# Kernel tuning notes

Measured on AMD Instinct MI355X. Metric: run time of the kernel, lower is better.

The kernel has to match this reference:

```python
import jax, jax.numpy as jnp
import numpy as np

N_NODES = 100000
N_EDGES = 1600000


def gcn_conv(x, row, col, norm, W, b, n_nodes):
    # PyG GCNConv: h = x @ W; aggregate normalized messages over (A + I); add bias
    h = x @ W                                   # [N, out]
    msg = h[col] * norm[:, None]                # [E+N, out] gather + scale
    out = jax.ops.segment_sum(msg, row, num_segments=n_nodes)  # scatter-add
    return out + b


def _norm_and_loops(edge_index, n_nodes):
    # add self-loops, compute symmetric normalization coefficients
    row = jnp.concatenate([edge_index[0], jnp.arange(n_nodes, dtype=edge_index.dtype)])
    col = jnp.concatenate([edge_index[1], jnp.arange(n_nodes, dtype=edge_index.dtype)])
    deg = jax.ops.segment_sum(jnp.ones_like(row, dtype=jnp.float32), row,
                              num_segments=n_nodes)
    dinv = jnp.where(deg > 0, jax.lax.rsqrt(deg), 0.0)
    norm = dinv[row] * dinv[col]
    return row, col, norm


def reference(x, edge_index, W1, b1, W2, b2, W3, b3):
    n_nodes = x.shape[0]
    row, col, norm = _norm_and_loops(edge_index, n_nodes)
    h = jax.nn.relu(gcn_conv(x, row, col, norm, W1, b1, n_nodes))
    h = jax.nn.relu(gcn_conv(h, row, col, norm, W2, b2, n_nodes))
    h = gcn_conv(h, row, col, norm, W3, b3, n_nodes)
    return jax.nn.log_softmax(h, axis=1)


def setup_inputs() -> dict:
    key = jax.random.key(0)
    ks = jax.random.split(key, 5)
    d_in, d_hid, d_out = 128, 128, 16
    x = jax.random.normal(ks[0], (N_NODES, d_in), dtype=jnp.float32)
    edge_index = jax.random.randint(ks[1], (2, N_EDGES), 0, N_NODES, dtype=jnp.int64)
    s1 = 1.0 / np.sqrt(d_in)
    s3 = 1.0 / np.sqrt(d_hid)
    W1 = jax.random.normal(ks[2], (d_in, d_hid), dtype=jnp.float32) * s1
    W2 = jax.random.normal(ks[3], (d_hid, d_hid), dtype=jnp.float32) * s3
    W3 = jax.random.normal(ks[4], (d_hid, d_out), dtype=jnp.float32) * s3
    return {
        "x": x, "edge_index": edge_index,
        "W1": W1, "b1": jnp.zeros((d_hid,), jnp.float32),
        "W2": W2, "b2": jnp.zeros((d_hid,), jnp.float32),
        "W3": W3, "b3": jnp.zeros((d_out,), jnp.float32),
    }
```

## Files before the change

kernel.cpp:

```cpp
#include <hip/hip_runtime.h>

typedef unsigned int u32;
typedef _Float16 f16;
typedef __attribute__((ext_vector_type(8))) _Float16 half8;
typedef __attribute__((ext_vector_type(2))) _Float16 half2_t;
typedef __attribute__((ext_vector_type(4))) float f32x4;

#define D_IN 128
#define D_HID 128
#define D_OUT 16
#define RPB 128
#define MAXBUCK 1024
#define CHUNK 16384
#define PGRAN 4
#define SLACK 2048


__global__ __launch_bounds__(256) void detect_k(const int* __restrict__ ei,
                                                u32* __restrict__ flag, int n) {
    int i = blockIdx.x * 256 + threadIdx.x;
    if (i < n && (i & 1) && ei[i] != 0) atomicOr(flag, 1u);
}

__device__ inline int load_row(const int* ei, u32 f, int e, int E) {
    return f ? ei[e] : ei[2 * e];
}
__device__ inline int load_col(const int* ei, u32 f, int e, int E) {
    return f ? ei[E + e] : ei[2 * E + 2 * e];
}
__device__ inline int clampi(int v, int n) {
    v = v < 0 ? 0 : v;
    return v >= n ? n - 1 : v;
}
__device__ inline u32 al16(u32 v) { return (v + 15u) & ~15u; }

__global__ __launch_bounds__(256) void hist_k(const int* __restrict__ ei,
                                              const u32* __restrict__ flag,
                                              u32* __restrict__ Hmat,
                                              int E, int N, int NBK, int NB) {
    __shared__ u32 lh[MAXBUCK];
    int tid = threadIdx.x;
    for (int i = tid; i < NBK; i += 256) lh[i] = 0;
    __syncthreads();
    u32 f = *flag;
    int base = blockIdx.x * CHUNK;
    int lim = base + CHUNK < E ? base + CHUNK : E;
    for (int e = base + tid; e < lim; e += 256) {
        int r = clampi(load_row(ei, f, e, E), N);
        atomicAdd(&lh[(u32)r >> 7], 1u);
    }
    __syncthreads();
    for (int i = tid; i < NBK; i += 256)
        Hmat[(size_t)i * NB + blockIdx.x] = lh[i];
}

__global__ __launch_bounds__(256) void scan1(const u32* __restrict__ cnt,
                                             u32* __restrict__ excl,
                                             u32* __restrict__ partial, int n) {
    __shared__ u32 sm[256];
    int tid = threadIdx.x;
    int i = blockIdx.x * 256 + tid;
    u32 v = (i < n) ? cnt[i] : 0u;
    sm[tid] = v;
    __syncthreads();
    for (int off = 1; off < 256; off <<= 1) {
        u32 t = (tid >= off) ? sm[tid - off] : 0u;
        __syncthreads();
        sm[tid] += t;
        __syncthreads();
    }
    if (i < n) excl[i] = sm[tid] - v;
    if (tid == 255) partial[blockIdx.x] = sm[255];
}

__global__ __launch_bounds__(512) void scan2(u32* __restrict__ partial, int nb) {
    __shared__ u32 sm[512];
    int tid = threadIdx.x;
    u32 v = (tid < nb) ? partial[tid] : 0u;
    sm[tid] = v;
    __syncthreads();
    for (int off = 1; off < 512; off <<= 1) {
        u32 t = (tid >= off) ? sm[tid - off] : 0u;
        __syncthreads();
        sm[tid] += t;
        __syncthreads();
    }
    if (tid < nb) partial[tid] = sm[tid] - v;
}

__global__ __launch_bounds__(256) void scan3(u32* __restrict__ excl,
                                             const u32* __restrict__ partial,
                                             int n, int E) {
    int i = blockIdx.x * 256 + threadIdx.x;
    if (i < n) excl[i] += partial[blockIdx.x];
    if (i == 0) excl[n] = (u32)E;
}

__global__ __launch_bounds__(256) void scatter_bd(const int* __restrict__ ei,
                                                  const u32* __restrict__ flag,
                                                  const u32* __restrict__ Hbase,
                                                  u32* __restrict__ bdata,
                                                  int E, int N, int NBK, int NB) {
    __shared__ u32 lbase[MAXBUCK];
    int tid = threadIdx.x;
    for (int i = tid; i < NBK; i += 256)
        lbase[i] = Hbase[(size_t)i * NB + blockIdx.x];
    __syncthreads();
    u32 f = *flag;
    int base = blockIdx.x * CHUNK;
    int lim = base + CHUNK < E ? base + CHUNK : E;
    for (int e = base + tid; e < lim; e += 256) {
        int r = clampi(load_row(ei, f, e, E), N);
        int c = clampi(load_col(ei, f, e, E), N);
        u32 pos = atomicAdd(&lbase[(u32)r >> 7], 1u);
        if (pos < (u32)E) bdata[pos] = ((u32)(r & (RPB - 1)) << 20) | (u32)c;
    }
}

__global__ __launch_bounds__(256) void finalize_k(const u32* __restrict__ bdata,
                                                  const u32* __restrict__ Hbase,
                                                  u32* __restrict__ row_start,
                                                  u32* __restrict__ rend,
                                                  float* __restrict__ dinv,
                                                  u32* __restrict__ ecol,
                                                  int N, int E, int NB) {
    __shared__ u32 smc[RPB];
    __shared__ u32 cur[RPB];
    int b = blockIdx.x;
    int tid = threadIdx.x;
    u32 s = Hbase[(size_t)b * NB];
    u32 t = Hbase[(size_t)(b + 1) * NB];
    u32 pbase = al16(s) + (u32)b * SLACK;
    if (tid < RPB) smc[tid] = 0;
    __syncthreads();
    for (u32 i = s + tid; i < t; i += 256)
        atomicAdd(&smc[bdata[i] >> 20], 1u);
    __syncthreads();
    u32 deg = (tid < RPB) ? smc[tid] : 0;
    u32 pdeg = (deg + PGRAN - 1) & ~(u32)(PGRAN - 1);
    if (tid < RPB) smc[tid] = pdeg;
    __syncthreads();
    for (int off = 1; off < RPB; off <<= 1) {
        u32 tv = (tid < RPB && tid >= off) ? smc[tid - off] : 0u;
        __syncthreads();
        if (tid < RPB) smc[tid] += tv;
        __syncthreads();
    }
    u32 pexcl = (tid < RPB) ? (smc[tid] - pdeg) : 0;
    if (tid < RPB) {
        int r = b * RPB + tid;
        if (r < N) {
            row_start[r] = pbase + pexcl;
            rend[r] = pbase + pexcl + pdeg;
            dinv[r] = rsqrtf((float)(deg + 1u));
        }
        cur[tid] = pbase + pexcl;
    }
    __syncthreads();
    for (u32 i = s + tid; i < t; i += 256) {
        u32 rec = bdata[i];
        u32 pos = atomicAdd(&cur[rec >> 20], 1u);
        ecol[pos] = rec & 0xFFFFFu;
    }
    __syncthreads();
    if (tid < RPB) {
        u32 st = pbase + pexcl;
        for (u32 k = deg; k < pdeg; k++) ecol[st + k] = (u32)N;
    }
}

__global__ __launch_bounds__(256) void reformat_all(const float* __restrict__ W1,
                                                    const float* __restrict__ W2,
                                                    const float* __restrict__ W3,
                                                    f16* __restrict__ W1h, f16* __restrict__ W1l,
                                                    f16* __restrict__ W2h, f16* __restrict__ W2l,
                                                    f16* __restrict__ W3h, f16* __restrict__ W3l,
                                                    f16* __restrict__ hzero,
                                                    f16* __restrict__ h3zero) {
    if (blockIdx.x == 17) {
        int tix = threadIdx.x;
        if (tix < 128) hzero[tix] = (f16)0;
        else if (tix < 144) h3zero[tix - 128] = (f16)0;
        return;
    }
    const float* W;
    f16 *Wh, *Wl;
    int ntiles, bidx;
    if (blockIdx.x < 8) { W = W1; Wh = W1h; Wl = W1l; ntiles = 8; bidx = blockIdx.x; }
    else if (blockIdx.x < 16) { W = W2; Wh = W2h; Wl = W2l; ntiles = 8; bidx = blockIdx.x - 8; }
    else { W = W3; Wh = W3h; Wl = W3l; ntiles = 1; bidx = 0; }
    int idx = bidx * 256 + threadIdx.x;
    int total = 4 * ntiles * 64;
    if (idx >= total) return;
    int lane = idx & 63;
    int st = idx >> 6;
    int t = st % ntiles;
    int s = st / ntiles;
    int Nc = ntiles * 16;
    int n = t * 16 + (lane & 15);
    int kb = lane >> 4;
    half8 vh, vl;
#pragma unroll
    for (int j = 0; j < 8; j++) {
        float w = W[(size_t)(s * 32 + kb * 8 + j) * Nc + n];
        f16 hi = (f16)w;
        f16 lo = (f16)(w - (float)hi);
        vh[j] = hi;
        vl[j] = lo;
    }
    *(half8*)(Wh + (size_t)idx * 8) = vh;
    *(half8*)(Wl + (size_t)idx * 8) = vl;
}


__global__ __launch_bounds__(256) void gemm128_l1(const float* __restrict__ A,
                                                  const f16* __restrict__ Wh,
                                                  const f16* __restrict__ Wl,
                                                  const float* __restrict__ dinv,
                                                  f16* __restrict__ H, int M) {
    int wave = threadIdx.x >> 6, lane = threadIdx.x & 63;
    int mbase = blockIdx.x * 64 + wave * 16;
    int mload = mbase + (lane & 15);
    if (mload >= M) mload = M - 1;
    int kq = lane >> 4;
    f32x4 acc[8];
#pragma unroll
    for (int t = 0; t < 8; t++) acc[t] = (f32x4){0.f, 0.f, 0.f, 0.f};
#pragma unroll
    for (int s = 0; s < 4; s++) {
        const float* ap = A + (size_t)mload * 128 + s * 32 + kq * 8;
        half8 ah, al;
#pragma unroll
        for (int j = 0; j < 8; j++) {
            float v = ap[j];
            f16 hi = (f16)v;
            ah[j] = hi;
            al[j] = (f16)(v - (float)hi);
        }
#pragma unroll
        for (int t = 0; t < 8; t++) {
            half8 bh = *(const half8*)(Wh + (size_t)((s * 8 + t) * 64 + lane) * 8);
            half8 bl = *(const half8*)(Wl + (size_t)((s * 8 + t) * 64 + lane) * 8);
            acc[t] = __builtin_amdgcn_mfma_f32_16x16x32_f16(ah, bh, acc[t], 0, 0, 0);
            acc[t] = __builtin_amdgcn_mfma_f32_16x16x32_f16(ah, bl, acc[t], 0, 0, 0);
            acc[t] = __builtin_amdgcn_mfma_f32_16x16x32_f16(al, bh, acc[t], 0, 0, 0);
        }
    }
    int coln = lane & 15;
    int rbase = mbase + ((lane >> 4) << 2);
    float dsc[4];
#pragma unroll
    for (int i = 0; i < 4; i++) {
        int rr = rbase + i;
        dsc[i] = dinv[rr < M ? rr : M - 1];
    }
#pragma unroll
    for (int t = 0; t < 8; t++) {
#pragma unroll
        for (int i = 0; i < 4; i++) {
            int rr = rbase + i;
            if (rr < M) H[(size_t)rr * 128 + t * 16 + coln] = (f16)(acc[t][i] * dsc[i]);
        }
    }
}

__global__ __launch_bounds__(256) void gemm128_l2(const f16* __restrict__ A,
                                                  const f16* __restrict__ Wh,
                                                  const f16* __restrict__ Wl,
                                                  f16* __restrict__ H, int M) {
    int wave = threadIdx.x >> 6, lane = threadIdx.x & 63;
    int mbase = blockIdx.x * 64 + wave * 16;
    int mload = mbase + (lane & 15);
    if (mload >= M) mload = M - 1;
    int kq = lane >> 4;
    f32x4 acc[8];
#pragma unroll
    for (int t = 0; t < 8; t++) acc[t] = (f32x4){0.f, 0.f, 0.f, 0.f};
#pragma unroll
    for (int s = 0; s < 4; s++) {
        half8 a = *(const half8*)(A + (size_t)mload * 128 + s * 32 + kq * 8);
#pragma unroll
        for (int t = 0; t < 8; t++) {
            half8 bh = *(const half8*)(Wh + (size_t)((s * 8 + t) * 64 + lane) * 8);
            half8 bl = *(const half8*)(Wl + (size_t)((s * 8 + t) * 64 + lane) * 8);
            acc[t] = __builtin_amdgcn_mfma_f32_16x16x32_f16(a, bh, acc[t], 0, 0, 0);
            acc[t] = __builtin_amdgcn_mfma_f32_16x16x32_f16(a, bl, acc[t], 0, 0, 0);
        }
    }
    int coln = lane & 15;
    int rbase = mbase + ((lane >> 4) << 2);
#pragma unroll
    for (int t = 0; t < 8; t++) {
#pragma unroll
        for (int i = 0; i < 4; i++) {
            int rr = rbase + i;
            if (rr < M) H[(size_t)rr * 128 + t * 16 + coln] = (f16)acc[t][i];
        }
    }
}

__global__ __launch_bounds__(256) void gemm16(const f16* __restrict__ A,
                                              const f16* __restrict__ Wh,
                                              const f16* __restrict__ Wl,
                                              f16* __restrict__ H, int M) {
    int wave = threadIdx.x >> 6, lane = threadIdx.x & 63;
    int mbase = blockIdx.x * 64 + wave * 16;
    int mload = mbase + (lane & 15);
    if (mload >= M) mload = M - 1;
    int kq = lane >> 4;
    f32x4 acc = (f32x4){0.f, 0.f, 0.f, 0.f};
#pragma unroll
    for (int s = 0; s < 4; s++) {
        half8 a = *(const half8*)(A + (size_t)mload * 128 + s * 32 + kq * 8);
        half8 bh = *(const half8*)(Wh + (size_t)(s * 64 + lane) * 8);
        half8 bl = *(const half8*)(Wl + (size_t)(s * 64 + lane) * 8);
        acc = __builtin_amdgcn_mfma_f32_16x16x32_f16(a, bh, acc, 0, 0, 0);
        acc = __builtin_amdgcn_mfma_f32_16x16x32_f16(a, bl, acc, 0, 0, 0);
    }
    int coln = lane & 15;
    int rbase = mbase + ((lane >> 4) << 2);
#pragma unroll
    for (int i = 0; i < 4; i++) {
        int rr = rbase + i;
        if (rr < M) H[(size_t)rr * 16 + coln] = (f16)acc[i];
    }
}

__global__ __launch_bounds__(256) void agg128(const f16* __restrict__ h,
                                              const u32* __restrict__ ecol,
                                              const u32* __restrict__ row_start,
                                              const u32* __restrict__ rend,
                                              const float* __restrict__ dinv,
                                              const float* __restrict__ bias,
                                              f16* __restrict__ out, int M) {
    int lane = threadIdx.x & 63;
    int wave = __builtin_amdgcn_readfirstlane(threadIdx.x >> 6);
    int r = blockIdx.x * 4 + wave;
    if (r >= M) return;
    u32 beg = (u32)__builtin_amdgcn_readfirstlane((int)row_start[r]);
    u32 end = (u32)__builtin_amdgcn_readfirstlane((int)rend[r]);
    float dr = dinv[r];
    const char* hb = (const char*)h;
    u32 loff = (u32)lane << 2;
    float ax0 = 0, ay0 = 0, ax1 = 0, ay1 = 0, ax2 = 0, ay2 = 0, ax3 = 0, ay3 = 0;
    u32 e = beg;
    for (; e + 16 <= end; e += 16) {
        const u32* ep = ecol + e;
        u32 c[16];
#pragma unroll
        for (int j = 0; j < 16; j++) c[j] = ep[j];
        half2_t v[16];
#pragma unroll
        for (int j = 0; j < 16; j++)
            v[j] = *(const half2_t*)(hb + ((c[j] << 8) + loff));
#pragma unroll
        for (int j = 0; j < 16; j += 4) {
            ax0 = fmaf((float)v[j][0],     dr, ax0); ay0 = fmaf((float)v[j][1],     dr, ay0);
            ax1 = fmaf((float)v[j + 1][0], dr, ax1); ay1 = fmaf((float)v[j + 1][1], dr, ay1);
            ax2 = fmaf((float)v[j + 2][0], dr, ax2); ay2 = fmaf((float)v[j + 2][1], dr, ay2);
            ax3 = fmaf((float)v[j + 3][0], dr, ax3); ay3 = fmaf((float)v[j + 3][1], dr, ay3);
        }
    }
    for (; e < end; e += 4) {
        const u32* ep = ecol + e;
        u32 c0 = ep[0], c1 = ep[1], c2 = ep[2], c3 = ep[3];
        half2_t v0 = *(const half2_t*)(hb + ((c0 << 8) + loff));
        half2_t v1 = *(const half2_t*)(hb + ((c1 << 8) + loff));
        half2_t v2 = *(const half2_t*)(hb + ((c2 << 8) + loff));
        half2_t v3 = *(const half2_t*)(hb + ((c3 << 8) + loff));
        ax0 = fmaf((float)v0[0], dr, ax0); ay0 = fmaf((float)v0[1], dr, ay0);
        ax1 = fmaf((float)v1[0], dr, ax1); ay1 = fmaf((float)v1[1], dr, ay1);
        ax2 = fmaf((float)v2[0], dr, ax2); ay2 = fmaf((float)v2[1], dr, ay2);
        ax3 = fmaf((float)v3[0], dr, ax3); ay3 = fmaf((float)v3[1], dr, ay3);
    }
    half2_t vs = *(const half2_t*)(hb + (((u32)r << 8) + loff));
    float2 bb = ((const float2*)bias)[lane];
    float ax = ((ax0 + ax1) + (ax2 + ax3)) + fmaf((float)vs[0], dr, bb.x);
    float ay = ((ay0 + ay1) + (ay2 + ay3)) + fmaf((float)vs[1], dr, bb.y);
    ax = fmaxf(ax, 0.f) * dr;
    ay = fmaxf(ay, 0.f) * dr;
    half2_t o;
    o[0] = (f16)ax;
    o[1] = (f16)ay;
    ((half2_t*)out)[(size_t)r * 64 + lane] = o;
}

__global__ __launch_bounds__(256) void agg16_lsm(const f16* __restrict__ h3,
                                                 const u32* __restrict__ ecol,
                                                 const u32* __restrict__ row_start,
                                                 const u32* __restrict__ rend,
                                                 const float* __restrict__ dinv,
                                                 const float* __restrict__ bias,
                                                 float* __restrict__ out, int M) {
    int g = threadIdx.x >> 4, l = threadIdx.x & 15;
    int r = blockIdx.x * 16 + g;
    if (r >= M) return;
    u32 beg = row_start[r], end = rend[r];
    float a0 = 0.f, a1 = 0.f, a2 = 0.f, a3 = 0.f;
    u32 e = beg;
    for (; e + 8 <= end; e += 8) {
        u32 c[8];
#pragma unroll
        for (int j = 0; j < 8; j++) c[j] = ecol[e + j];
        f16 v[8];
#pragma unroll
        for (int j = 0; j < 8; j++) v[j] = h3[(size_t)c[j] * 16 + l];
        a0 += (float)v[0] + (float)v[4];
        a1 += (float)v[1] + (float)v[5];
        a2 += (float)v[2] + (float)v[6];
        a3 += (float)v[3] + (float)v[7];
    }
    if (e < end) {
        u32 c[4];
#pragma unroll
        for (int j = 0; j < 4; j++) c[j] = ecol[e + j];
        f16 v[4];
#pragma unroll
        for (int j = 0; j < 4; j++) v[j] = h3[(size_t)c[j] * 16 + l];
        a0 += (float)v[0];
        a1 += (float)v[1];
        a2 += (float)v[2];
        a3 += (float)v[3];
    }
    float dr = dinv[r];
    float acc = (((a0 + a1) + (a2 + a3)) + (float)h3[(size_t)r * 16 + l]) * dr +
                bias[l];
    float m = acc;
#pragma unroll
    for (int o = 8; o >= 1; o >>= 1) m = fmaxf(m, __shfl_xor(m, o, 16));
    float ex = expf(acc - m);
    float s = ex;
#pragma unroll
    for (int o = 8; o >= 1; o >>= 1) s += __shfl_xor(s, o, 16);
    out[(size_t)r * 16 + l] = acc - m - logf(s);
}


extern "C" void kernel_launch(void* const* d_in, const int* in_sizes, int n_in,
                              void* d_out, int out_size, void* d_ws, size_t ws_size,
                              hipStream_t stream) {
    const float* x = (const float*)d_in[0];
    const int* ei = (const int*)d_in[1];
    const float* W1 = (const float*)d_in[2];
    const float* b1 = (const float*)d_in[3];
    const float* W2 = (const float*)d_in[4];
    const float* b2 = (const float*)d_in[5];
    const float* W3 = (const float*)d_in[6];
    const float* b3 = (const float*)d_in[7];
    int N = in_sizes[0] / D_IN;
    int E = in_sizes[1] / 2;

    int NBK = (N + RPB - 1) / RPB;
    int NB = (E + CHUNK - 1) / CHUNK;
    int L = NBK * NB;
    size_t Epad = ((size_t)E + 16) + (size_t)NBK * SLACK + 256;

    char* p = (char*)d_ws;
    auto alloc = [&](size_t bytes) -> void* {
        void* q = (void*)p;
        p += (bytes + 255) & ~(size_t)255;
        return q;
    };
    u32* flag = (u32*)alloc(256);
    float* dinv = (float*)alloc((size_t)N * 4);
    u32* row_start = (u32*)alloc((size_t)(N + 1) * 4);
    u32* rend = (u32*)alloc((size_t)N * 4);
    u32* partial2 = (u32*)alloc(4096);
    u32* Hmat = (u32*)alloc((size_t)(L + 1) * 4);
    u32* ecol = (u32*)alloc(Epad * 4);
    u32* bdata = (u32*)alloc((size_t)E * 4);
    f16* wf1h = (f16*)alloc(16384 * 2);
    f16* wf1l = (f16*)alloc(16384 * 2);
    f16* wf2h = (f16*)alloc(16384 * 2);
    f16* wf2l = (f16*)alloc(16384 * 2);
    f16* wf3h = (f16*)alloc(2048 * 2);
    f16* wf3l = (f16*)alloc(2048 * 2);
    f16* h = (f16*)alloc((size_t)(N + 1) * 128 * 2);
    f16* act = (f16*)alloc((size_t)N * 128 * 2);
    f16* h3 = (f16*)alloc((size_t)(N + 1) * 16 * 2);
    (void)ws_size; (void)n_in; (void)out_size;

    hipMemsetAsync(flag, 0, 4, stream);

    int nb2 = (L + 255) / 256;

    detect_k<<<32, 256, 0, stream>>>(ei, flag, 8192);
    hist_k<<<NB, 256, 0, stream>>>(ei, flag, Hmat, E, N, NBK, NB);
    scan1<<<nb2, 256, 0, stream>>>(Hmat, Hmat, partial2, L);
    scan2<<<1, 512, 0, stream>>>(partial2, nb2);
    scan3<<<nb2, 256, 0, stream>>>(Hmat, partial2, L, E);
    scatter_bd<<<NB, 256, 0, stream>>>(ei, flag, Hmat, bdata, E, N, NBK, NB);
    finalize_k<<<NBK, 256, 0, stream>>>(bdata, Hmat, row_start, rend, dinv,
                                        ecol, N, E, NB);

    reformat_all<<<18, 256, 0, stream>>>(W1, W2, W3, wf1h, wf1l, wf2h, wf2l,
                                         wf3h, wf3l,
                                         h + (size_t)N * 128,
                                         h3 + (size_t)N * 16);

    int gb = (N + 63) / 64;
    int ab = (N + 3) / 4;
    gemm128_l1<<<gb, 256, 0, stream>>>(x, wf1h, wf1l, dinv, h, N);
    agg128<<<ab, 256, 0, stream>>>(h, ecol, row_start, rend, dinv, b1, act, N);
    gemm128_l2<<<gb, 256, 0, stream>>>(act, wf2h, wf2l, h, N);
    agg128<<<ab, 256, 0, stream>>>(h, ecol, row_start, rend, dinv, b2, act, N);
    gemm16<<<gb, 256, 0, stream>>>(act, wf3h, wf3l, h3, N);
    agg16_lsm<<<(N + 15) / 16, 256, 0, stream>>>(h3, ecol, row_start, rend,
                                                 dinv, b3, (float*)d_out, N);
}
```

Baseline: 383.3 us.

## Stage GEMM weights in LDS, batch edge loads, pack row descriptors

Several independent tweaks. The hist and scatter kernels use a smaller CHUNK and unroll four edge loads per iteration to raise memory-level parallelism. The three GEMM kernels copy the split-f16 weights into shared memory and hoist activation loads ahead of the MFMA loop. Row start and end are packed into one uint2 descriptor, and the self and bias loads in the aggregation kernels are moved earlier. The trade-off is heavy LDS use in the 128-wide GEMMs (64KB per block), which may reduce occupancy.

```diff
diff --git a/kernel.cpp b/kernel.cpp
--- a/kernel.cpp
+++ b/kernel.cpp
@@ -11,7 +11,7 @@
 #define D_OUT 16
 #define RPB 128
 #define MAXBUCK 1024
-#define CHUNK 16384
+#define CHUNK 10240
 #define PGRAN 4
 #define SLACK 2048
 
@@ -45,9 +45,16 @@
     u32 f = *flag;
     int base = blockIdx.x * CHUNK;
     int lim = base + CHUNK < E ? base + CHUNK : E;
-    for (int e = base + tid; e < lim; e += 256) {
-        int r = clampi(load_row(ei, f, e, E), N);
-        atomicAdd(&lh[(u32)r >> 7], 1u);
+    for (int e = base + tid; e < lim; e += 1024) {
+        int e1 = e + 256, e2 = e + 512, e3 = e + 768;
+        int r0 = clampi(load_row(ei, f, e, E), N);
+        int r1 = (e1 < lim) ? clampi(load_row(ei, f, e1, E), N) : -1;
+        int r2 = (e2 < lim) ? clampi(load_row(ei, f, e2, E), N) : -1;
+        int r3 = (e3 < lim) ? clampi(load_row(ei, f, e3, E), N) : -1;
+        atomicAdd(&lh[(u32)r0 >> 7], 1u);
+        if (r1 >= 0) atomicAdd(&lh[(u32)r1 >> 7], 1u);
+        if (r2 >= 0) atomicAdd(&lh[(u32)r2 >> 7], 1u);
+        if (r3 >= 0) atomicAdd(&lh[(u32)r3 >> 7], 1u);
     }
     __syncthreads();
     for (int i = tid; i < NBK; i += 256)
@@ -109,18 +116,34 @@
     u32 f = *flag;
     int base = blockIdx.x * CHUNK;
     int lim = base + CHUNK < E ? base + CHUNK : E;
-    for (int e = base + tid; e < lim; e += 256) {
-        int r = clampi(load_row(ei, f, e, E), N);
-        int c = clampi(load_col(ei, f, e, E), N);
-        u32 pos = atomicAdd(&lbase[(u32)r >> 7], 1u);
-        if (pos < (u32)E) bdata[pos] = ((u32)(r & (RPB - 1)) << 20) | (u32)c;
+    for (int e = base + tid; e < lim; e += 1024) {
+        int e1 = e + 256, e2 = e + 512, e3 = e + 768;
+        int r0 = clampi(load_row(ei, f, e, E), N);
+        int c0 = clampi(load_col(ei, f, e, E), N);
+        int r1 = -1, c1 = 0, r2 = -1, c2 = 0, r3 = -1, c3 = 0;
+        if (e1 < lim) { r1 = clampi(load_row(ei, f, e1, E), N); c1 = clampi(load_col(ei, f, e1, E), N); }
+        if (e2 < lim) { r2 = clampi(load_row(ei, f, e2, E), N); c2 = clampi(load_col(ei, f, e2, E), N); }
+        if (e3 < lim) { r3 = clampi(load_row(ei, f, e3, E), N); c3 = clampi(load_col(ei, f, e3, E), N); }
+        u32 pos = atomicAdd(&lbase[(u32)r0 >> 7], 1u);
+        if (pos < (u32)E) bdata[pos] = ((u32)(r0 & (RPB - 1)) << 20) | (u32)c0;
+        if (r1 >= 0) {
+            pos = atomicAdd(&lbase[(u32)r1 >> 7], 1u);
+            if (pos < (u32)E) bdata[pos] = ((u32)(r1 & (RPB - 1)) << 20) | (u32)c1;
+        }
+        if (r2 >= 0) {
+            pos = atomicAdd(&lbase[(u32)r2 >> 7], 1u);
+            if (pos < (u32)E) bdata[pos] = ((u32)(r2 & (RPB - 1)) << 20) | (u32)c2;
+        }
+        if (r3 >= 0) {
+            pos = atomicAdd(&lbase[(u32)r3 >> 7], 1u);
+            if (pos < (u32)E) bdata[pos] = ((u32)(r3 & (RPB - 1)) << 20) | (u32)c3;
+        }
     }
 }
 
 __global__ __launch_bounds__(256) void finalize_k(const u32* __restrict__ bdata,
                                                   const u32* __restrict__ Hbase,
-                                                  u32* __restrict__ row_start,
-                                                  u32* __restrict__ rend,
+                                                  uint2* __restrict__ rdesc,
                                                   float* __restrict__ dinv,
                                                   u32* __restrict__ ecol,
                                                   int N, int E, int NB) {
@@ -150,8 +173,7 @@
     if (tid < RPB) {
         int r = b * RPB + tid;
         if (r < N) {
-            row_start[r] = pbase + pexcl;
-            rend[r] = pbase + pexcl + pdeg;
+            rdesc[r] = make_uint2(pbase + pexcl, pbase + pexcl + pdeg);
             dinv[r] = rsqrtf((float)(deg + 1u));
         }
         cur[tid] = pbase + pexcl;
@@ -218,29 +240,46 @@
                                                   const f16* __restrict__ Wl,
                                                   const float* __restrict__ dinv,
                                                   f16* __restrict__ H, int M) {
+    __shared__ f16 sBh[2048 * 8];
+    __shared__ f16 sBl[2048 * 8];
+    for (int i = threadIdx.x; i < 2048; i += 256) {
+        *(half8*)(sBh + (size_t)i * 8) = *(const half8*)(Wh + (size_t)i * 8);
+        *(half8*)(sBl + (size_t)i * 8) = *(const half8*)(Wl + (size_t)i * 8);
+    }
     int wave = threadIdx.x >> 6, lane = threadIdx.x & 63;
     int mbase = blockIdx.x * 64 + wave * 16;
     int mload = mbase + (lane & 15);
     if (mload >= M) mload = M - 1;
     int kq = lane >> 4;
-    f32x4 acc[8];
-#pragma unroll
-    for (int t = 0; t < 8; t++) acc[t] = (f32x4){0.f, 0.f, 0.f, 0.f};
+    f32x4 a0[4], a1[4];
 #pragma unroll
     for (int s = 0; s < 4; s++) {
         const float* ap = A + (size_t)mload * 128 + s * 32 + kq * 8;
+        a0[s] = *(const f32x4*)ap;
+        a1[s] = *(const f32x4*)(ap + 4);
+    }
+    f32x4 acc[8];
+#pragma unroll
+    for (int t = 0; t < 8; t++) acc[t] = (f32x4){0.f, 0.f, 0.f, 0.f};
+    __syncthreads();
+#pragma unroll
+    for (int s = 0; s < 4; s++) {
         half8 ah, al;
 #pragma unroll
-        for (int j = 0; j < 8; j++) {
-            float v = ap[j];
+        for (int j = 0; j < 4; j++) {
+            float v = a0[s][j];
             f16 hi = (f16)v;
             ah[j] = hi;
             al[j] = (f16)(v - (float)hi);
+            float w = a1[s][j];
+            f16 wi = (f16)w;
+            ah[j + 4] = wi;
+            al[j + 4] = (f16)(w - (float)wi);
         }
 #pragma unroll
         for (int t = 0; t < 8; t++) {
-            half8 bh = *(const half8*)(Wh + (size_t)((s * 8 + t) * 64 + lane) * 8);
-            half8 bl = *(const half8*)(Wl + (size_t)((s * 8 + t) * 64 + lane) * 8);
+            half8 bh = *(const half8*)(sBh + (size_t)((s * 8 + t) * 64 + lane) * 8);
+            half8 bl = *(const half8*)(sBl + (size_t)((s * 8 + t) * 64 + lane) * 8);
             acc[t] = __builtin_amdgcn_mfma_f32_16x16x32_f16(ah, bh, acc[t], 0, 0, 0);
             acc[t] = __builtin_amdgcn_mfma_f32_16x16x32_f16(ah, bl, acc[t], 0, 0, 0);
             acc[t] = __builtin_amdgcn_mfma_f32_16x16x32_f16(al, bh, acc[t], 0, 0, 0);
@@ -268,23 +307,33 @@
                                                   const f16* __restrict__ Wh,
                                                   const f16* __restrict__ Wl,
                                                   f16* __restrict__ H, int M) {
+    __shared__ f16 sBh[2048 * 8];
+    __shared__ f16 sBl[2048 * 8];
+    for (int i = threadIdx.x; i < 2048; i += 256) {
+        *(half8*)(sBh + (size_t)i * 8) = *(const half8*)(Wh + (size_t)i * 8);
+        *(half8*)(sBl + (size_t)i * 8) = *(const half8*)(Wl + (size_t)i * 8);
+    }
     int wave = threadIdx.x >> 6, lane = threadIdx.x & 63;
     int mbase = blockIdx.x * 64 + wave * 16;
     int mload = mbase + (lane & 15);
     if (mload >= M) mload = M - 1;
     int kq = lane >> 4;
+    half8 a[4];
+#pragma unroll
+    for (int s = 0; s < 4; s++)
+        a[s] = *(const half8*)(A + (size_t)mload * 128 + s * 32 + kq * 8);
     f32x4 acc[8];
 #pragma unroll
     for (int t = 0; t < 8; t++) acc[t] = (f32x4){0.f, 0.f, 0.f, 0.f};
+    __syncthreads();
 #pragma unroll
     for (int s = 0; s < 4; s++) {
-        half8 a = *(const half8*)(A + (size_t)mload * 128 + s * 32 + kq * 8);
 #pragma unroll
         for (int t = 0; t < 8; t++) {
-            half8 bh = *(const half8*)(Wh + (size_t)((s * 8 + t) * 64 + lane) * 8);
-            half8 bl = *(const half8*)(Wl + (size_t)((s * 8 + t) * 64 + lane) * 8);
-            acc[t] = __builtin_amdgcn_mfma_f32_16x16x32_f16(a, bh, acc[t], 0, 0, 0);
-            acc[t] = __builtin_amdgcn_mfma_f32_16x16x32_f16(a, bl, acc[t], 0, 0, 0);
+            half8 bh = *(const half8*)(sBh + (size_t)((s * 8 + t) * 64 + lane) * 8);
+            half8 bl = *(const half8*)(sBl + (size_t)((s * 8 + t) * 64 + lane) * 8);
+            acc[t] = __builtin_amdgcn_mfma_f32_16x16x32_f16(a[s], bh, acc[t], 0, 0, 0);
+            acc[t] = __builtin_amdgcn_mfma_f32_16x16x32_f16(a[s], bl, acc[t], 0, 0, 0);
         }
     }
     int coln = lane & 15;
@@ -303,19 +352,30 @@
                                               const f16* __restrict__ Wh,
                                               const f16* __restrict__ Wl,
                                               f16* __restrict__ H, int M) {
+    __shared__ f16 sBh[256 * 8];
+    __shared__ f16 sBl[256 * 8];
+    if (threadIdx.x < 256) {
+        int i = threadIdx.x;
+        *(half8*)(sBh + (size_t)i * 8) = *(const half8*)(Wh + (size_t)i * 8);
+        *(half8*)(sBl + (size_t)i * 8) = *(const half8*)(Wl + (size_t)i * 8);
+    }
     int wave = threadIdx.x >> 6, lane = threadIdx.x & 63;
     int mbase = blockIdx.x * 64 + wave * 16;
     int mload = mbase + (lane & 15);
     if (mload >= M) mload = M - 1;
     int kq = lane >> 4;
+    half8 a[4];
+#pragma unroll
+    for (int s = 0; s < 4; s++)
+        a[s] = *(const half8*)(A + (size_t)mload * 128 + s * 32 + kq * 8);
     f32x4 acc = (f32x4){0.f, 0.f, 0.f, 0.f};
+    __syncthreads();
 #pragma unroll
     for (int s = 0; s < 4; s++) {
-        half8 a = *(const half8*)(A + (size_t)mload * 128 + s * 32 + kq * 8);
-        half8 bh = *(const half8*)(Wh + (size_t)(s * 64 + lane) * 8);
-        half8 bl = *(const half8*)(Wl + (size_t)(s * 64 + lane) * 8);
-        acc = __builtin_amdgcn_mfma_f32_16x16x32_f16(a, bh, acc, 0, 0, 0);
-        acc = __builtin_amdgcn_mfma_f32_16x16x32_f16(a, bl, acc, 0, 0, 0);
+        half8 bh = *(const half8*)(sBh + (size_t)(s * 64 + lane) * 8);
+        half8 bl = *(const half8*)(sBl + (size_t)(s * 64 + lane) * 8);
+        acc = __builtin_amdgcn_mfma_f32_16x16x32_f16(a[s], bh, acc, 0, 0, 0);
+        acc = __builtin_amdgcn_mfma_f32_16x16x32_f16(a[s], bl, acc, 0, 0, 0);
     }
     int coln = lane & 15;
     int rbase = mbase + ((lane >> 4) << 2);
@@ -328,8 +388,7 @@
 
 __global__ __launch_bounds__(256) void agg128(const f16* __restrict__ h,
                                               const u32* __restrict__ ecol,
-                                              const u32* __restrict__ row_start,
-                                              const u32* __restrict__ rend,
+                                              const uint2* __restrict__ rdesc,
                                               const float* __restrict__ dinv,
                                               const float* __restrict__ bias,
                                               f16* __restrict__ out, int M) {
@@ -337,13 +396,15 @@
     int wave = __builtin_amdgcn_readfirstlane(threadIdx.x >> 6);
     int r = blockIdx.x * 4 + wave;
     if (r >= M) return;
-    u32 beg = (u32)__builtin_amdgcn_readfirstlane((int)row_start[r]);
-    u32 end = (u32)__builtin_amdgcn_readfirstlane((int)rend[r]);
+    uint2 d = rdesc[r];
+    u32 e = (u32)__builtin_amdgcn_readfirstlane((int)d.x);
+    u32 end = (u32)__builtin_amdgcn_readfirstlane((int)d.y);
     float dr = dinv[r];
     const char* hb = (const char*)h;
     u32 loff = (u32)lane << 2;
+    float2 bb = ((const float2*)bias)[lane];
+    half2_t vs = *(const half2_t*)(hb + (((u32)r << 8) + loff));
     float ax0 = 0, ay0 = 0, ax1 = 0, ay1 = 0, ax2 = 0, ay2 = 0, ax3 = 0, ay3 = 0;
-    u32 e = beg;
     for (; e + 16 <= end; e += 16) {
         const u32* ep = ecol + e;
         u32 c[16];
@@ -373,8 +434,6 @@
         ax2 = fmaf((float)v2[0], dr, ax2); ay2 = fmaf((float)v2[1], dr, ay2);
         ax3 = fmaf((float)v3[0], dr, ax3); ay3 = fmaf((float)v3[1], dr, ay3);
     }
-    half2_t vs = *(const half2_t*)(hb + (((u32)r << 8) + loff));
-    float2 bb = ((const float2*)bias)[lane];
     float ax = ((ax0 + ax1) + (ax2 + ax3)) + fmaf((float)vs[0], dr, bb.x);
     float ay = ((ay0 + ay1) + (ay2 + ay3)) + fmaf((float)vs[1], dr, bb.y);
     ax = fmaxf(ax, 0.f) * dr;
@@ -387,15 +446,18 @@
 
 __global__ __launch_bounds__(256) void agg16_lsm(const f16* __restrict__ h3,
                                                  const u32* __restrict__ ecol,
-                                                 const u32* __restrict__ row_start,
-                                                 const u32* __restrict__ rend,
+                                                 const uint2* __restrict__ rdesc,
                                                  const float* __restrict__ dinv,
                                                  const float* __restrict__ bias,
                                                  float* __restrict__ out, int M) {
     int g = threadIdx.x >> 4, l = threadIdx.x & 15;
     int r = blockIdx.x * 16 + g;
     if (r >= M) return;
-    u32 beg = row_start[r], end = rend[r];
+    uint2 d = rdesc[r];
+    u32 beg = d.x, end = d.y;
+    float dr = dinv[r];
+    float bl = bias[l];
+    float self = (float)h3[(size_t)r * 16 + l];
     float a0 = 0.f, a1 = 0.f, a2 = 0.f, a3 = 0.f;
     u32 e = beg;
     for (; e + 8 <= end; e += 8) {
@@ -422,9 +484,7 @@
         a2 += (float)v[2];
         a3 += (float)v[3];
     }
-    float dr = dinv[r];
-    float acc = (((a0 + a1) + (a2 + a3)) + (float)h3[(size_t)r * 16 + l]) * dr +
-                bias[l];
+    float acc = (((a0 + a1) + (a2 + a3)) + self) * dr + bl;
     float m = acc;
 #pragma unroll
     for (int o = 8; o >= 1; o >>= 1) m = fmaxf(m, __shfl_xor(m, o, 16));
@@ -463,8 +523,7 @@
     };
     u32* flag = (u32*)alloc(256);
     float* dinv = (float*)alloc((size_t)N * 4);
-    u32* row_start = (u32*)alloc((size_t)(N + 1) * 4);
-    u32* rend = (u32*)alloc((size_t)N * 4);
+    uint2* rdesc = (uint2*)alloc((size_t)(N + 1) * 8);
     u32* partial2 = (u32*)alloc(4096);
     u32* Hmat = (u32*)alloc((size_t)(L + 1) * 4);
     u32* ecol = (u32*)alloc(Epad * 4);
@@ -490,8 +549,7 @@
     scan2<<<1, 512, 0, stream>>>(partial2, nb2);
     scan3<<<nb2, 256, 0, stream>>>(Hmat, partial2, L, E);
     scatter_bd<<<NB, 256, 0, stream>>>(ei, flag, Hmat, bdata, E, N, NBK, NB);
-    finalize_k<<<NBK, 256, 0, stream>>>(bdata, Hmat, row_start, rend, dinv,
-                                        ecol, N, E, NB);
+    finalize_k<<<NBK, 256, 0, stream>>>(bdata, Hmat, rdesc, dinv, ecol, N, E, NB);
 
     reformat_all<<<18, 256, 0, stream>>>(W1, W2, W3, wf1h, wf1l, wf2h, wf2l,
                                          wf3h, wf3l,
@@ -501,10 +559,10 @@
     int gb = (N + 63) / 64;
     int ab = (N + 3) / 4;
     gemm128_l1<<<gb, 256, 0, stream>>>(x, wf1h, wf1l, dinv, h, N);
-    agg128<<<ab, 256, 0, stream>>>(h, ecol, row_start, rend, dinv, b1, act, N);
+    agg128<<<ab, 256, 0, stream>>>(h, ecol, rdesc, dinv, b1, act, N);
     gemm128_l2<<<gb, 256, 0, stream>>>(act, wf2h, wf2l, h, N);
-    agg128<<<ab, 256, 0, stream>>>(h, ecol, row_start, rend, dinv, b2, act, N);
+    agg128<<<ab, 256, 0, stream>>>(h, ecol, rdesc, dinv, b2, act, N);
     gemm16<<<gb, 256, 0, stream>>>(act, wf3h, wf3l, h3, N);
-    agg16_lsm<<<(N + 15) / 16, 256, 0, stream>>>(h3, ecol, row_start, rend,
+    agg16_lsm<<<(N + 15) / 16, 256, 0, stream>>>(h3, ecol, rdesc,
                                                  dinv, b3, (float*)d_out, N);
 }
```

After: 336.2 us. 1.14x faster.
